# Performance work log

Measured on AMD Instinct MI355X. Metric: run time of the kernel, lower is better.

The kernel has to match this reference:

```python
import jax, jax.numpy as jnp
import numpy as np

B, D, N, F, O = 4096, 256, 128, 128, 256


def setup_inputs() -> dict:
    key = jax.random.key(0)
    ks = jax.random.split(key, 6)
    return {
        "x": jax.random.normal(ks[0], (B, D), dtype=jnp.float32),
        "node_weight": jax.random.normal(ks[1], (N, D + F, F), dtype=jnp.float32),  # torch.randn init
        "node_bias": jax.random.normal(ks[2], (N, F), dtype=jnp.float32),
        "attention": jax.random.normal(ks[3], (N, N), dtype=jnp.float32),
        "out_w": jax.random.normal(ks[4], (F, O), dtype=jnp.float32) * 0.05,  # Linear weight (transposed conv.)
        "out_b": jax.random.normal(ks[5], (O,), dtype=jnp.float32) * 0.05,
        "num_iterations": 3,
    }


def reference(x, node_weight, node_bias, attention, out_w, out_b, num_iterations):
    # connections[i, j] = softmax over j of attention row i
    conn = jax.nn.softmax(attention, axis=1)  # [N, N]
    # Split per-node weight: first F rows act on aggregated states, last D rows on x.
    W_s = node_weight[:, :F, :]   # [N, F, F]
    W_x = node_weight[:, F:, :]   # [N, D, F]
    # x contribution is identical every iteration; precompute once.
    xW = jnp.einsum('bd,ndf->nbf', x, W_x) + node_bias[:, None, :]  # [N, B, F]

    states0 = jnp.zeros((N, B, F), dtype=x.dtype)

    def step(states, _):
        agg = jnp.einsum('ij,jbf->ibf', conn, states)            # attention-weighted aggregation
        new = jax.nn.relu(jnp.einsum('nbf,nfg->nbg', agg, W_s) + xW)
        return new, None

    states, _ = jax.lax.scan(step, states0, None, length=num_iterations)
    final_state = states.mean(axis=0)                            # [B, F]
    return final_state @ out_w + out_b                           # [B, O]
```

## Files before the change

### kernel.cpp

```cpp
#include <hip/hip_runtime.h>

#define DEV __device__ __forceinline__

typedef __attribute__((ext_vector_type(8))) short short8;
typedef __attribute__((ext_vector_type(4))) float floatx4;
typedef __attribute__((ext_vector_type(4))) unsigned short ushort4v;
typedef __attribute__((ext_vector_type(8))) unsigned short ushort8v;

#define Bz 4096
#define Dz 256
#define Nz 128
#define Fz 128
#define Oz 256

static constexpr size_t OFF_CONN = 0;
static constexpr size_t OFF_WT   = 65536;
static constexpr size_t SZ_WT    = (size_t)Nz * 128 * 384 * 2;
static constexpr size_t OFF_OWT  = OFF_WT + SZ_WT;
static constexpr size_t OFF_XB   = OFF_OWT + 65536;
static constexpr size_t OFF_FIN  = OFF_XB + (size_t)Bz * Dz * 2;
static constexpr size_t OFF_ST   = OFF_FIN + (size_t)Bz * Fz * 2;

DEV unsigned short f2bf(float x) {
    unsigned u = __float_as_uint(x);
    u = (u + 0x7FFFu + ((u >> 16) & 1u)) >> 16;
    return (unsigned short)u;
}
DEV float bf2f(unsigned short h) {
    return __uint_as_float(((unsigned)h) << 16);
}

typedef const __attribute__((address_space(1))) void cglobal_void;
typedef __attribute__((address_space(3))) void lds_void;

DEV void gld_lds16(const void* g, void* l) {
    __builtin_amdgcn_global_load_lds((cglobal_void*)g, (lds_void*)l, 16, 0, 0);
}

__global__ __launch_bounds__(64) void k_softmax(const float* __restrict__ att,
                                                unsigned short* __restrict__ conn) {
    int i = blockIdx.x, t = threadIdx.x;
    float a0 = att[i * 128 + t];
    float a1 = att[i * 128 + 64 + t];
    float m = fmaxf(a0, a1);
    for (int o = 32; o > 0; o >>= 1) m = fmaxf(m, __shfl_down(m, o));
    m = __shfl(m, 0);
    float e0 = __expf(a0 - m), e1 = __expf(a1 - m);
    float s = e0 + e1;
    for (int o = 32; o > 0; o >>= 1) s += __shfl_down(s, o);
    s = __shfl(s, 0);
    float inv = 1.f / s;
    conn[i * 128 + t] = f2bf(e0 * inv);
    conn[i * 128 + 64 + t] = f2bf(e1 * inv);
}

__global__ __launch_bounds__(256) void k_transpose(const float* __restrict__ src,
                                                   unsigned short* __restrict__ dst,
                                                   int R, int C, int tilesC,
                                                   long sBatch, long dBatch) {
    __shared__ float ld[32][36];
    int tiles = (R / 32) * tilesC;
    int batch = blockIdx.x / tiles;
    int rem = blockIdx.x % tiles;
    int rt = rem / tilesC, ct = rem % tilesC;
    int t = threadIdx.x;
    int kr = t >> 3, c4 = (t & 7) * 4;
    float4 v = *(const float4*)&src[(size_t)batch * sBatch + (size_t)(rt * 32 + kr) * C + ct * 32 + c4];
    ld[kr][c4 + 0] = v.x; ld[kr][c4 + 1] = v.y; ld[kr][c4 + 2] = v.z; ld[kr][c4 + 3] = v.w;
    __syncthreads();
    int cr = kr, k4 = c4;
    ushort4v o;
    o[0] = f2bf(ld[k4 + 0][cr]);
    o[1] = f2bf(ld[k4 + 1][cr]);
    o[2] = f2bf(ld[k4 + 2][cr]);
    o[3] = f2bf(ld[k4 + 3][cr]);
    *(ushort4v*)&dst[(size_t)batch * dBatch + (size_t)(ct * 32 + cr) * R + rt * 32 + k4] = o;
}

__global__ __launch_bounds__(256) void k_convert(const float* __restrict__ src,
                                                 unsigned short* __restrict__ dst) {
    size_t idx = ((size_t)blockIdx.x * 256 + threadIdx.x) * 4;
    float4 v = *(const float4*)&src[idx];
    ushort4v o;
    o[0] = f2bf(v.x); o[1] = f2bf(v.y); o[2] = f2bf(v.z); o[3] = f2bf(v.w);
    *(ushort4v*)&dst[idx] = o;
}

__global__ __launch_bounds__(256) void k2_agg(const unsigned short* __restrict__ conn,
                                              unsigned short* __restrict__ ST) {
    __shared__ unsigned short lA[128 * 136];
    __shared__ unsigned short lB[32 * 128];
    int b = blockIdx.x;
    int t = threadIdx.x, wid = t >> 6, lane = t & 63, q = lane >> 4, cc = lane & 15;
    int wm = (wid >> 1) << 6, wn = (wid & 1) << 6;

#pragma unroll
    for (int it = 0; it < 8; it++) {
        int g = it * 256 + t;
        int row = g >> 4, cg = g & 15;
        *(short8*)&lA[row * 136 + cg * 8] = *(const short8*)&conn[row * 128 + cg * 8];
    }
    floatx4 acc[4][4];
#pragma unroll
    for (int mt = 0; mt < 4; mt++)
#pragma unroll
        for (int nt = 0; nt < 4; nt++) acc[mt][nt] = (floatx4){0.f, 0.f, 0.f, 0.f};

    for (int kt = 0; kt < 4; kt++) {
#pragma unroll
        for (int it = 0; it < 2; it++) {
            int g = it * 256 + t;
            int j = g >> 4, fg = g & 15;
            int lofs = __builtin_amdgcn_readfirstlane((it * 256 + (wid << 6)) * 8);
            gld_lds16(ST + ((size_t)(kt * 32 + j) * Bz + b) * Fz + fg * 8, lB + lofs);
        }
        __syncthreads();
        short8 af[4];
#pragma unroll
        for (int mt = 0; mt < 4; mt++)
            af[mt] = *(const short8*)&lA[(wm + mt * 16 + cc) * 136 + kt * 32 + q * 8];
        short8 bf[4];
#pragma unroll
        for (int nt = 0; nt < 4; nt++) {
            short8 v;
#pragma unroll
            for (int e = 0; e < 8; e++)
                v[e] = (short)lB[(q * 8 + e) * 128 + wn + nt * 16 + cc];
            bf[nt] = v;
        }
#pragma unroll
        for (int mt = 0; mt < 4; mt++)
#pragma unroll
            for (int nt = 0; nt < 4; nt++)
                acc[mt][nt] = __builtin_amdgcn_mfma_f32_16x16x32_bf16(af[mt], bf[nt], acc[mt][nt], 0, 0, 0);
        __syncthreads();
    }
#pragma unroll
    for (int mt = 0; mt < 4; mt++) {
#pragma unroll
        for (int nt = 0; nt < 4; nt++) {
            int f = wn + nt * 16 + cc;
#pragma unroll
            for (int r = 0; r < 4; r++) {
                int i = wm + mt * 16 + q * 4 + r;
                ST[((size_t)i * Bz + b) * Fz + f] = f2bf(acc[mt][nt][r]);
            }
        }
    }
}

template <int KT0>
__global__ __launch_bounds__(256) void k3_fused(unsigned short* __restrict__ ST,
                                                const unsigned short* __restrict__ XB,
                                                const unsigned short* __restrict__ WT,
                                                const float* __restrict__ nb) {
    __shared__ unsigned short lA[128 * 32];
    __shared__ unsigned short lB[128 * 32];
    int n = blockIdx.x >> 5, bt = blockIdx.x & 31;
    int t = threadIdx.x, wid = t >> 6, lane = t & 63, q = lane >> 4, cc = lane & 15;
    int wm = (wid >> 1) << 6, wn = (wid & 1) << 6;

    const unsigned short* Sg = ST + ((size_t)n * Bz + bt * 128) * Fz;
    const unsigned short* Xg = XB + (size_t)bt * 128 * Dz;
    const unsigned short* Bg = WT + (size_t)n * 128 * 384;

    floatx4 acc[4][4];
#pragma unroll
    for (int mt = 0; mt < 4; mt++)
#pragma unroll
        for (int nt = 0; nt < 4; nt++) acc[mt][nt] = (floatx4){0.f, 0.f, 0.f, 0.f};

    for (int kt = KT0; kt < 12; kt++) {
#pragma unroll
        for (int it = 0; it < 2; it++) {
            int g = it * 256 + t;
            int row = g >> 2, kg = g & 3;
            int lofs = __builtin_amdgcn_readfirstlane((it * 256 + (wid << 6)) * 8);
            if (kt < 4)
                gld_lds16(Sg + (size_t)row * Fz + kt * 32 + kg * 8, lA + lofs);
            else
                gld_lds16(Xg + (size_t)row * Dz + (kt - 4) * 32 + kg * 8, lA + lofs);
            gld_lds16(Bg + (size_t)row * 384 + kt * 32 + kg * 8, lB + lofs);
        }
        __syncthreads();
        short8 af[4], bfr[4];
#pragma unroll
        for (int mt = 0; mt < 4; mt++)
            af[mt] = *(const short8*)&lA[(wm + mt * 16 + cc) * 32 + q * 8];
#pragma unroll
        for (int nt = 0; nt < 4; nt++)
            bfr[nt] = *(const short8*)&lB[(wn + nt * 16 + cc) * 32 + q * 8];
#pragma unroll
        for (int mt = 0; mt < 4; mt++)
#pragma unroll
            for (int nt = 0; nt < 4; nt++)
                acc[mt][nt] = __builtin_amdgcn_mfma_f32_16x16x32_bf16(af[mt], bfr[nt], acc[mt][nt], 0, 0, 0);
        __syncthreads();
    }

#pragma unroll
    for (int nt = 0; nt < 4; nt++) {
        int f = wn + nt * 16 + cc;
        float bias = nb[n * Fz + f];
#pragma unroll
        for (int mt = 0; mt < 4; mt++) {
#pragma unroll
            for (int r = 0; r < 4; r++) {
                int b = bt * 128 + wm + mt * 16 + q * 4 + r;
                size_t off = ((size_t)n * Bz + b) * Fz + f;
                float v = acc[mt][nt][r] + bias;
                ST[off] = f2bf(v > 0.f ? v : 0.f);
            }
        }
    }
}

__global__ __launch_bounds__(256) void k4_mean(const unsigned short* __restrict__ S,
                                               unsigned short* __restrict__ fin) {
    int t = threadIdx.x;
    size_t base = (size_t)blockIdx.x * 2048 + (size_t)t * 8;
    float a[8] = {0.f, 0.f, 0.f, 0.f, 0.f, 0.f, 0.f, 0.f};
    for (int n = 0; n < Nz; n++) {
        ushort8v v = *(const ushort8v*)&S[(size_t)n * Bz * Fz + base];
#pragma unroll
        for (int e = 0; e < 8; e++) a[e] += bf2f(v[e]);
    }
    ushort8v o;
#pragma unroll
    for (int e = 0; e < 8; e++) o[e] = f2bf(a[e] * (1.f / 128.f));
    *(ushort8v*)&fin[base] = o;
}

__global__ __launch_bounds__(256) void k5_out(const unsigned short* __restrict__ fin,
                                              const unsigned short* __restrict__ owt,
                                              const float* __restrict__ ob,
                                              float* __restrict__ out) {
    __shared__ unsigned short lA[128 * 32];
    __shared__ unsigned short lB[128 * 32];
    int bt = blockIdx.x >> 1, ct = blockIdx.x & 1;
    int t = threadIdx.x, wid = t >> 6, lane = t & 63, q = lane >> 4, cc = lane & 15;
    int wm = (wid >> 1) << 6, wn = (wid & 1) << 6;

    const unsigned short* Ag = fin + (size_t)bt * 128 * Fz;
    const unsigned short* Bg = owt + (size_t)ct * 128 * Fz;

    floatx4 acc[4][4];
#pragma unroll
    for (int mt = 0; mt < 4; mt++)
#pragma unroll
        for (int nt = 0; nt < 4; nt++) acc[mt][nt] = (floatx4){0.f, 0.f, 0.f, 0.f};

    for (int kt = 0; kt < 4; kt++) {
#pragma unroll
        for (int it = 0; it < 2; it++) {
            int g = it * 256 + t;
            int row = g >> 2, kg = g & 3;
            int lofs = __builtin_amdgcn_readfirstlane((it * 256 + (wid << 6)) * 8);
            gld_lds16(Ag + (size_t)row * Fz + kt * 32 + kg * 8, lA + lofs);
            gld_lds16(Bg + (size_t)row * Fz + kt * 32 + kg * 8, lB + lofs);
        }
        __syncthreads();
        short8 af[4], bfr[4];
#pragma unroll
        for (int mt = 0; mt < 4; mt++)
            af[mt] = *(const short8*)&lA[(wm + mt * 16 + cc) * 32 + q * 8];
#pragma unroll
        for (int nt = 0; nt < 4; nt++)
            bfr[nt] = *(const short8*)&lB[(wn + nt * 16 + cc) * 32 + q * 8];
#pragma unroll
        for (int mt = 0; mt < 4; mt++)
#pragma unroll
            for (int nt = 0; nt < 4; nt++)
                acc[mt][nt] = __builtin_amdgcn_mfma_f32_16x16x32_bf16(af[mt], bfr[nt], acc[mt][nt], 0, 0, 0);
        __syncthreads();
    }
#pragma unroll
    for (int nt = 0; nt < 4; nt++) {
        int o = ct * 128 + wn + nt * 16 + cc;
        float bias = ob[o];
#pragma unroll
        for (int mt = 0; mt < 4; mt++) {
#pragma unroll
            for (int r = 0; r < 4; r++) {
                int b = bt * 128 + wm + mt * 16 + q * 4 + r;
                out[(size_t)b * Oz + o] = acc[mt][nt][r] + bias;
            }
        }
    }
}

extern "C" void kernel_launch(void* const* d_in, const int* in_sizes, int n_in,
                              void* d_out, int out_size, void* d_ws, size_t ws_size,
                              hipStream_t stream) {
    const float* x = (const float*)d_in[0];
    const float* nw = (const float*)d_in[1];
    const float* nb = (const float*)d_in[2];
    const float* att = (const float*)d_in[3];
    const float* ow = (const float*)d_in[4];
    const float* ob = (const float*)d_in[5];
    char* ws = (char*)d_ws;
    unsigned short* CONN = (unsigned short*)(ws + OFF_CONN);
    unsigned short* WT = (unsigned short*)(ws + OFF_WT);
    unsigned short* OWT = (unsigned short*)(ws + OFF_OWT);
    unsigned short* XB = (unsigned short*)(ws + OFF_XB);
    unsigned short* FIN = (unsigned short*)(ws + OFF_FIN);
    unsigned short* ST = (unsigned short*)(ws + OFF_ST);
    float* out = (float*)d_out;

    k_softmax<<<Nz, 64, 0, stream>>>(att, CONN);
    k_transpose<<<Nz * 48, 256, 0, stream>>>(nw, WT, 384, 128, 4, (long)384 * 128, (long)128 * 384);
    k_transpose<<<32, 256, 0, stream>>>(ow, OWT, 128, 256, 8, 0, 0);
    k_convert<<<(Bz * Dz) / 1024, 256, 0, stream>>>(x, XB);

    k3_fused<4><<<Nz * 32, 256, 0, stream>>>(ST, XB, WT, nb);

    for (int it = 0; it < 2; it++) {
        k2_agg<<<Bz, 256, 0, stream>>>(CONN, ST);
        k3_fused<0><<<Nz * 32, 256, 0, stream>>>(ST, XB, WT, nb);
    }

    k4_mean<<<(Bz * Fz) / 2048, 256, 0, stream>>>(ST, FIN);
    k5_out<<<64, 256, 0, stream>>>(FIN, OWT, ob, out);
}
```

Measured before the change: 443.9 us.

## Double-buffer LDS staging and coalesce epilogue stores via swizzled LDS in agg and fused kernels

Both the aggregation and fused GEMM kernels now use two LDS buffers, prefetching the next K tiles with async global-to-LDS loads while the current tile runs through MFMA. Explicit vmcnt waits and raw barriers replace __syncthreads. The epilogues, which previously wrote scattered 2-byte values to global memory, now write results into a XOR-swizzled LDS tile and then issue 16-byte coalesced stores. This targets load latency and uncoalesced write traffic, at the cost of more LDS per block, which may lower occupancy, and hand-counted waitcnt values that must match the number of loads in flight.

```diff
diff --git a/kernel.cpp b/kernel.cpp
--- a/kernel.cpp
+++ b/kernel.cpp
@@ -89,7 +89,7 @@
 __global__ __launch_bounds__(256) void k2_agg(const unsigned short* __restrict__ conn,
                                               unsigned short* __restrict__ ST) {
     __shared__ unsigned short lA[128 * 136];
-    __shared__ unsigned short lB[32 * 128];
+    __shared__ unsigned short lB[2][32 * 128];
     int b = blockIdx.x;
     int t = threadIdx.x, wid = t >> 6, lane = t & 63, q = lane >> 4, cc = lane & 15;
     int wm = (wid >> 1) << 6, wn = (wid & 1) << 6;
@@ -106,15 +106,25 @@
 #pragma unroll
         for (int nt = 0; nt < 4; nt++) acc[mt][nt] = (floatx4){0.f, 0.f, 0.f, 0.f};
 
-    for (int kt = 0; kt < 4; kt++) {
+    auto STG = [&](int bufi, int kt) {
 #pragma unroll
         for (int it = 0; it < 2; it++) {
             int g = it * 256 + t;
             int j = g >> 4, fg = g & 15;
             int lofs = __builtin_amdgcn_readfirstlane((it * 256 + (wid << 6)) * 8);
-            gld_lds16(ST + ((size_t)(kt * 32 + j) * Bz + b) * Fz + fg * 8, lB + lofs);
-        }
-        __syncthreads();
+            gld_lds16(ST + ((size_t)(kt * 32 + j) * Bz + b) * Fz + fg * 8, &lB[bufi][0] + lofs);
+        }
+    };
+    STG(0, 0);
+    STG(1, 1);
+
+#pragma unroll
+    for (int kt = 0; kt < 4; kt++) {
+        int cur = kt & 1;
+        if (kt < 3) asm volatile("s_waitcnt vmcnt(2) lgkmcnt(0)" ::: "memory");
+        else        asm volatile("s_waitcnt vmcnt(0) lgkmcnt(0)" ::: "memory");
+        __builtin_amdgcn_s_barrier();
+        __builtin_amdgcn_sched_barrier(0);
         short8 af[4];
 #pragma unroll
         for (int mt = 0; mt < 4; mt++)
@@ -125,7 +135,7 @@
             short8 v;
 #pragma unroll
             for (int e = 0; e < 8; e++)
-                v[e] = (short)lB[(q * 8 + e) * 128 + wn + nt * 16 + cc];
+                v[e] = (short)lB[cur][(q * 8 + e) * 128 + wn + nt * 16 + cc];
             bf[nt] = v;
         }
 #pragma unroll
@@ -133,19 +143,30 @@
 #pragma unroll
             for (int nt = 0; nt < 4; nt++)
                 acc[mt][nt] = __builtin_amdgcn_mfma_f32_16x16x32_bf16(af[mt], bf[nt], acc[mt][nt], 0, 0, 0);
-        __syncthreads();
-    }
-#pragma unroll
-    for (int mt = 0; mt < 4; mt++) {
+        __builtin_amdgcn_sched_barrier(0);
+        __builtin_amdgcn_s_barrier();
+        if (kt + 2 < 4) STG(cur, kt + 2);
+    }
+
+#pragma unroll
+    for (int mt = 0; mt < 4; mt++)
 #pragma unroll
         for (int nt = 0; nt < 4; nt++) {
             int f = wn + nt * 16 + cc;
 #pragma unroll
             for (int r = 0; r < 4; r++) {
-                int i = wm + mt * 16 + q * 4 + r;
-                ST[((size_t)i * Bz + b) * Fz + f] = f2bf(acc[mt][nt][r]);
+                int il = wm + mt * 16 + q * 4 + r;
+                lA[il * 128 + (f ^ ((il & 7) << 3))] = f2bf(acc[mt][nt][r]);
             }
         }
+    __syncthreads();
+#pragma unroll
+    for (int it = 0; it < 8; it++) {
+        int idx = it * 256 + t;
+        int il = idx >> 4, ch = idx & 15;
+        int sch = ch ^ (il & 7);
+        ushort8v v = *(const ushort8v*)&lA[il * 128 + sch * 8];
+        *(ushort8v*)&ST[((size_t)il * Bz + b) * Fz + ch * 8] = v;
     }
 }
 
@@ -154,8 +175,7 @@
                                                 const unsigned short* __restrict__ XB,
                                                 const unsigned short* __restrict__ WT,
                                                 const float* __restrict__ nb) {
-    __shared__ unsigned short lA[128 * 32];
-    __shared__ unsigned short lB[128 * 32];
+    __shared__ unsigned short lds[2][2][128 * 32];
     int n = blockIdx.x >> 5, bt = blockIdx.x & 31;
     int t = threadIdx.x, wid = t >> 6, lane = t & 63, q = lane >> 4, cc = lane & 15;
     int wm = (wid >> 1) << 6, wn = (wid & 1) << 6;
@@ -170,34 +190,47 @@
 #pragma unroll
         for (int nt = 0; nt < 4; nt++) acc[mt][nt] = (floatx4){0.f, 0.f, 0.f, 0.f};
 
-    for (int kt = KT0; kt < 12; kt++) {
+    auto STAGE = [&](int bufi, int kt) {
 #pragma unroll
         for (int it = 0; it < 2; it++) {
             int g = it * 256 + t;
             int row = g >> 2, kg = g & 3;
             int lofs = __builtin_amdgcn_readfirstlane((it * 256 + (wid << 6)) * 8);
             if (kt < 4)
-                gld_lds16(Sg + (size_t)row * Fz + kt * 32 + kg * 8, lA + lofs);
+                gld_lds16(Sg + (size_t)row * Fz + kt * 32 + kg * 8, &lds[bufi][0][0] + lofs);
             else
-                gld_lds16(Xg + (size_t)row * Dz + (kt - 4) * 32 + kg * 8, lA + lofs);
-            gld_lds16(Bg + (size_t)row * 384 + kt * 32 + kg * 8, lB + lofs);
-        }
-        __syncthreads();
+                gld_lds16(Xg + (size_t)row * Dz + (kt - 4) * 32 + kg * 8, &lds[bufi][0][0] + lofs);
+            gld_lds16(Bg + (size_t)row * 384 + kt * 32 + kg * 8, &lds[bufi][1][0] + lofs);
+        }
+    };
+    STAGE(0, KT0);
+    STAGE(1, KT0 + 1);
+
+#pragma unroll
+    for (int kt = KT0; kt < 12; kt++) {
+        int cur = (kt - KT0) & 1;
+        if (kt < 11) asm volatile("s_waitcnt vmcnt(4) lgkmcnt(0)" ::: "memory");
+        else         asm volatile("s_waitcnt vmcnt(0) lgkmcnt(0)" ::: "memory");
+        __builtin_amdgcn_s_barrier();
+        __builtin_amdgcn_sched_barrier(0);
         short8 af[4], bfr[4];
 #pragma unroll
         for (int mt = 0; mt < 4; mt++)
-            af[mt] = *(const short8*)&lA[(wm + mt * 16 + cc) * 32 + q * 8];
+            af[mt] = *(const short8*)&lds[cur][0][(wm + mt * 16 + cc) * 32 + q * 8];
 #pragma unroll
         for (int nt = 0; nt < 4; nt++)
-            bfr[nt] = *(const short8*)&lB[(wn + nt * 16 + cc) * 32 + q * 8];
+            bfr[nt] = *(const short8*)&lds[cur][1][(wn + nt * 16 + cc) * 32 + q * 8];
 #pragma unroll
         for (int mt = 0; mt < 4; mt++)
 #pragma unroll
             for (int nt = 0; nt < 4; nt++)
                 acc[mt][nt] = __builtin_amdgcn_mfma_f32_16x16x32_bf16(af[mt], bfr[nt], acc[mt][nt], 0, 0, 0);
-        __syncthreads();
-    }
-
+        __builtin_amdgcn_sched_barrier(0);
+        __builtin_amdgcn_s_barrier();
+        if (kt + 2 < 12) STAGE(cur, kt + 2);
+    }
+
+    unsigned short* outT = &lds[0][0][0];
 #pragma unroll
     for (int nt = 0; nt < 4; nt++) {
         int f = wn + nt * 16 + cc;
@@ -206,12 +239,21 @@
         for (int mt = 0; mt < 4; mt++) {
 #pragma unroll
             for (int r = 0; r < 4; r++) {
-                int b = bt * 128 + wm + mt * 16 + q * 4 + r;
-                size_t off = ((size_t)n * Bz + b) * Fz + f;
+                int bl = wm + mt * 16 + q * 4 + r;
                 float v = acc[mt][nt][r] + bias;
-                ST[off] = f2bf(v > 0.f ? v : 0.f);
+                outT[bl * 128 + (f ^ ((bl & 7) << 3))] = f2bf(v > 0.f ? v : 0.f);
             }
         }
+    }
+    __syncthreads();
+    size_t base = ((size_t)n * Bz + (size_t)bt * 128) * Fz;
+#pragma unroll
+    for (int it = 0; it < 8; it++) {
+        int idx = it * 256 + t;
+        int bl = idx >> 4, ch = idx & 15;
+        int sch = ch ^ (bl & 7);
+        ushort8v v = *(const ushort8v*)&outT[bl * 128 + sch * 8];
+        *(ushort8v*)&ST[base + (size_t)idx * 8] = v;
     }
 }
 
```

After: 404.9 us. 1.1x faster.
